# Kernel optimization log

Measured on AMD Instinct MI355X. Metric: run time of the kernel, lower is better.

## Reference

```python
import jax, jax.numpy as jnp
import numpy as np

N_NODES = 100000
N_EDGES = 3200000
DIM = 128
N_LAYERS = 3
NUM_GRAPHS = 128
BN_EPS = 1e-5
GIN_EPS = 0.0  # eps buffer initialized to 0, train_eps=False


def setup_inputs() -> dict:
    key = jax.random.key(0)
    ks = jax.random.split(key, 12)
    s = 1.0 / np.sqrt(DIM)
    inp = {
        "x": jax.random.normal(ks[0], (N_NODES, DIM), jnp.float32),
        "edge_index": jax.random.randint(ks[1], (2, N_EDGES), 0, N_NODES, jnp.int64),
        "batch": jnp.sort(jax.random.randint(ks[2], (N_NODES,), 0, NUM_GRAPHS, jnp.int64)),
        # node encoder Linear(x_dim, emb_dim)
        "W_node": jax.random.uniform(ks[3], (DIM, DIM), jnp.float32, -s, s),
        "b_node": jax.random.uniform(ks[4], (DIM,), jnp.float32, -s, s),
        # per-layer MLP: Linear -> BatchNorm -> ReLU -> Linear, stacked over layers
        "W1": jax.random.uniform(ks[5], (N_LAYERS, DIM, DIM), jnp.float32, -s, s),
        "b1": jax.random.uniform(ks[6], (N_LAYERS, DIM), jnp.float32, -s, s),
        "gamma": jnp.ones((N_LAYERS, DIM), jnp.float32),
        "beta": jnp.zeros((N_LAYERS, DIM), jnp.float32),
        "W2": jax.random.uniform(ks[7], (N_LAYERS, DIM, DIM), jnp.float32, -s, s),
        "b2": jax.random.uniform(ks[8], (N_LAYERS, DIM), jnp.float32, -s, s),
    }
    return inp


def _batchnorm(y, gamma, beta):
    # training-mode batch statistics over the node dimension (biased variance)
    mean = jnp.mean(y, axis=0)
    var = jnp.mean(jnp.square(y - mean), axis=0)
    return (y - mean) * jax.lax.rsqrt(var + BN_EPS) * gamma + beta


def reference(x, edge_index, batch, W_node, b_node, W1, b1, gamma, beta, W2, b2):
    src, dst = edge_index[0], edge_index[1]
    n = x.shape[0]
    h = x @ W_node + b_node  # [N, D]
    for i in range(N_LAYERS):
        # GINConv: scatter-add gathered neighbor features, eps-residual, MLP
        agg = jax.ops.segment_sum(h[src], dst, num_segments=n)  # [N, D]
        out = agg + (1.0 + GIN_EPS) * h
        y = out @ W1[i] + b1[i]
        y = jax.nn.relu(_batchnorm(y, gamma[i], beta[i]))
        y = y @ W2[i] + b2[i]
        h = jax.nn.relu(y)  # outer ReLU in Encoder.forward (dropout_p=0)
    # global_add_pool
    return jax.ops.segment_sum(h, batch, num_segments=NUM_GRAPHS)  # [G, D]
```

## Files before the change

kernel.cpp:

```cpp
#include <hip/hip_runtime.h>

#define N_NODES 100000
#define M_PAD   100096
#define N_EDGES 3200000
#define DIM 128
#define N_LAYERS 3
#define NUM_GRAPHS 128
#define BN_EPS 1e-5f

#define DST_SHIFT 7
#define BUCKET_NODES 128
#define N_BUCKETS ((N_NODES + BUCKET_NODES - 1) / BUCKET_NODES)
#define BUCKET_CAP 4864
#define EDGES_PER_BLOCK 16384
#define BIN_BLOCKS ((N_EDGES + EDGES_PER_BLOCK - 1) / EDGES_PER_BLOCK)
#define N_BANDS 64

#define AGG_BLOCKS 25000
#define AGG_CHUNK  (AGG_BLOCKS / 8)

typedef unsigned int uint32;
typedef unsigned short u16;
typedef __attribute__((ext_vector_type(8))) short bf16x8;
typedef __attribute__((ext_vector_type(4))) float f32x4;

__device__ __forceinline__ float bf2f(u16 u) {
    union { uint32 i; float f; } c;
    c.i = ((uint32)u) << 16;
    return c.f;
}
__device__ __forceinline__ u16 f2bf(float f) {
    union { float f; uint32 i; } c;
    c.f = f;
    uint32 i = c.i;
    return (u16)((i + 0x7FFFu + ((i >> 16) & 1u)) >> 16);
}
__device__ __forceinline__ float lo_bf(uint32 v) {
    union { uint32 i; float f; } c;
    c.i = v << 16;
    return c.f;
}
__device__ __forceinline__ float hi_bf(uint32 v) {
    union { uint32 i; float f; } c;
    c.i = v & 0xFFFF0000u;
    return c.f;
}
__device__ __forceinline__ uint32 pack_bf2(float a, float b) {
    return ((uint32)f2bf(b) << 16) | (uint32)f2bf(a);
}
__device__ __forceinline__ void unpack_add8(float* acc, uint4 v) {
    acc[0] += lo_bf(v.x); acc[1] += hi_bf(v.x);
    acc[2] += lo_bf(v.y); acc[3] += hi_bf(v.y);
    acc[4] += lo_bf(v.z); acc[5] += hi_bf(v.z);
    acc[6] += lo_bf(v.w); acc[7] += hi_bf(v.w);
}

__global__ __launch_bounds__(256) void zero_misc(int* __restrict__ gcur,
                                                 float* __restrict__ bn_stats,
                                                 float* __restrict__ outp,
                                                 uint32* __restrict__ aggpad32) {
    int i = blockIdx.x * 256 + threadIdx.x;
    if (i < N_BUCKETS) gcur[i] = 0;
    if (i < N_LAYERS * 2 * DIM) bn_stats[i] = 0.f;
    if (i < NUM_GRAPHS * DIM) outp[i] = 0.f;
    if (i < (M_PAD - N_NODES) * DIM / 2) aggpad32[i] = 0;
}

__global__ __launch_bounds__(256) void bin_by_dst(const int* __restrict__ src,
                                                  const int* __restrict__ dst,
                                                  int* __restrict__ gcur,
                                                  uint32* __restrict__ packed) {
    __shared__ int cnt[N_BUCKETS];
    __shared__ int cur[N_BUCKETS];
    int t = threadIdx.x;
    int e0 = blockIdx.x * EDGES_PER_BLOCK;
    for (int i = t; i < N_BUCKETS; i += 256) cnt[i] = 0;
    __syncthreads();

    for (int j = 0; j < EDGES_PER_BLOCK / 256; ++j) {
        int e = e0 + j * 256 + t;
        if (e < N_EDGES) atomicAdd(&cnt[dst[e] >> DST_SHIFT], 1);
    }
    __syncthreads();
    for (int i = t; i < N_BUCKETS; i += 256) {
        int c = cnt[i];
        cur[i] = c ? atomicAdd(&gcur[i], c) : 0;
    }
    __syncthreads();
    for (int j = 0; j < EDGES_PER_BLOCK / 256; ++j) {
        int e = e0 + j * 256 + t;
        if (e < N_EDGES) {
            int d = dst[e];
            int b = d >> DST_SHIFT;
            int pos = atomicAdd(&cur[b], 1);
            if (pos < BUCKET_CAP)
                packed[(size_t)b * BUCKET_CAP + pos] =
                    (uint32)src[e] | ((uint32)(d & (BUCKET_NODES - 1)) << 17);
        }
    }
}

__global__ void scan_buckets(const int* __restrict__ gcur, int* __restrict__ obase,
                             int* __restrict__ row_ptr) {
    __shared__ int s[N_BUCKETS];
    int t = threadIdx.x;
    for (int i = t; i < N_BUCKETS; i += 256) {
        int c = gcur[i];
        s[i] = (c > BUCKET_CAP) ? BUCKET_CAP : c;
    }
    __syncthreads();
    if (t == 0) {
        int run = 0;
        for (int i = 0; i < N_BUCKETS; ++i) {
            int c = s[i];
            s[i] = run;
            run += c;
        }
        row_ptr[N_NODES] = run;
    }
    __syncthreads();
    for (int i = t; i < N_BUCKETS; i += 256) obase[i] = s[i];
}

__global__ __launch_bounds__(256) void build_buckets(const uint32* __restrict__ packed,
                                                     const int* __restrict__ gcur,
                                                     const int* __restrict__ obase_arr,
                                                     int* __restrict__ row_ptr,
                                                     int* __restrict__ col_src) {
    __shared__ uint32 ed[BUCKET_CAP];
    __shared__ uint32 ed2[BUCKET_CAP];
    __shared__ int bandcur[N_BANDS];
    __shared__ int ncnt[BUCKET_NODES];
    __shared__ int ncur[BUCKET_NODES];
    int b = blockIdx.x, t = threadIdx.x;
    int cnt = gcur[b];
    if (cnt > BUCKET_CAP) cnt = BUCKET_CAP;
    int obase = obase_arr[b];
    int n0 = b * BUCKET_NODES;

    if (t < N_BANDS) bandcur[t] = 0;
    if (t < BUCKET_NODES) ncnt[t] = 0;
    __syncthreads();

    const uint32* reg = packed + (size_t)b * BUCKET_CAP;
    for (int i = t; i < cnt; i += 256) {
        uint32 v = reg[i];
        ed[i] = v;
        atomicAdd(&bandcur[(v & 0x1FFFFu) >> 11], 1);
        atomicAdd(&ncnt[v >> 17], 1);
    }
    __syncthreads();

    if (t == 0) {
        int run = 0;
        for (int w = 0; w < N_BANDS; ++w) {
            int c = bandcur[w];
            bandcur[w] = run;
            run += c;
        }
    }
    int myc = (t < BUCKET_NODES) ? ncnt[t] : 0;
    if (t < BUCKET_NODES) ncur[t] = myc;
    __syncthreads();
    for (int off = 1; off < BUCKET_NODES; off <<= 1) {
        int v = 0;
        if (t < BUCKET_NODES && t >= off) v = ncur[t - off];
        __syncthreads();
        if (t < BUCKET_NODES) ncur[t] += v;
        __syncthreads();
    }
    if (t < BUCKET_NODES) {
        int excl = ncur[t] - myc;
        ncur[t] = excl;
        int gn = n0 + t;
        if (gn < N_NODES) row_ptr[gn] = obase + excl;
    }
    __syncthreads();

    for (int i = t; i < cnt; i += 256) {
        uint32 v = ed[i];
        int p = atomicAdd(&bandcur[(v & 0x1FFFFu) >> 11], 1);
        ed2[p] = v;
    }
    __syncthreads();

    for (int i = t; i < cnt; i += 256) {
        uint32 v = ed2[i];
        int slot = atomicAdd(&ncur[v >> 17], 1);
        col_src[obase + slot] = (int)(v & 0x1FFFFu);
    }
}

__global__ void cvt_wt_all(const float* __restrict__ Wn, const float* __restrict__ W1,
                           const float* __restrict__ W2, u16* __restrict__ WT) {
    int m = blockIdx.x >> 7, n = blockIdx.x & 127, k = threadIdx.x;
    const float* src = (m == 0) ? Wn
                     : (m <= 3) ? W1 + (size_t)(m - 1) * DIM * DIM
                                : W2 + (size_t)(m - 4) * DIM * DIM;
    int L = n * 256 + k * 2;
    int Ls = L ^ ((n & 7) << 4);
    *(u16*)((char*)WT + (size_t)m * 32768 + Ls) = f2bf(src[(size_t)k * DIM + n]);
}

__global__ __launch_bounds__(256) void aggregate_bf(const u16* __restrict__ h,
                                                    const int* __restrict__ row_ptr,
                                                    const int* __restrict__ col_src,
                                                    u16* __restrict__ agg) {
    int wg = (blockIdx.x & 7) * AGG_CHUNK + (blockIdx.x >> 3);
    int wv = wg * 4 + (threadIdx.x >> 6);
    int lane = threadIdx.x & 63;
    int q = lane >> 4, c = lane & 15;
    if (wv >= N_NODES) return;
    int beg = row_ptr[wv], end = row_ptr[wv + 1];
    const uint4* h4 = (const uint4*)h;

    float acc[8];
#pragma unroll
    for (int j = 0; j < 8; ++j) acc[j] = 0.f;

    if (q == 0) {
        uint4 v = h4[(size_t)wv * 16 + c];
        unpack_add8(acc, v);
    }
    int e = beg + q;
    for (; e + 12 < end; e += 16) {
        int i0 = col_src[e];
        int i1 = col_src[e + 4];
        int i2 = col_src[e + 8];
        int i3 = col_src[e + 12];
        uint4 v0 = h4[(size_t)i0 * 16 + c];
        uint4 v1 = h4[(size_t)i1 * 16 + c];
        uint4 v2 = h4[(size_t)i2 * 16 + c];
        uint4 v3 = h4[(size_t)i3 * 16 + c];
        unpack_add8(acc, v0);
        unpack_add8(acc, v1);
        unpack_add8(acc, v2);
        unpack_add8(acc, v3);
    }
    for (; e < end; e += 4) {
        uint4 v0 = h4[(size_t)col_src[e] * 16 + c];
        unpack_add8(acc, v0);
    }
#pragma unroll
    for (int j = 0; j < 8; ++j) {
        acc[j] += __shfl_xor(acc[j], 16);
        acc[j] += __shfl_xor(acc[j], 32);
    }
    if (q == 0) {
        uint4 o;
        o.x = pack_bf2(acc[0], acc[1]);
        o.y = pack_bf2(acc[2], acc[3]);
        o.z = pack_bf2(acc[4], acc[5]);
        o.w = pack_bf2(acc[6], acc[7]);
        *(uint4*)&agg[(size_t)wv * DIM + c * 8] = o;
    }
}

template <int MODE>
__global__ __launch_bounds__(256) void gemm_v2(const void* __restrict__ Av,
                                               const u16* __restrict__ WTs,
                                               const float* __restrict__ bias,
                                               u16* __restrict__ outp,
                                               float* __restrict__ bn_sum,
                                               float* __restrict__ bn_sumsq,
                                               const float* __restrict__ gamma,
                                               const float* __restrict__ beta) {
    __shared__ u16 sB[DIM * DIM];
    __shared__ float sc_[DIM];
    __shared__ float sh_[DIM];
    __shared__ float ls[4][DIM];
    __shared__ float lq[4][DIM];

    int t = threadIdx.x;
    int wid = t >> 6, lane = t & 63;
    int hw = lane >> 4, c = lane & 15;
    int row0 = blockIdx.x * 128 + wid * 32;

    bf16x8 a[2][4];
    float4 af[2][4][2];
#pragma unroll
    for (int rf = 0; rf < 2; ++rf) {
        int row = row0 + rf * 16 + c;
#pragma unroll
        for (int ks = 0; ks < 4; ++ks) {
            int k0 = ks * 32 + hw * 8;
            if (MODE == 0) {
                const float* xf = (const float*)Av;
                af[rf][ks][0] = make_float4(0.f, 0.f, 0.f, 0.f);
                af[rf][ks][1] = af[rf][ks][0];
                if (row < N_NODES) {
                    af[rf][ks][0] = *(const float4*)&xf[(size_t)row * DIM + k0];
                    af[rf][ks][1] = *(const float4*)&xf[(size_t)row * DIM + k0 + 4];
                }
            } else {
                const u16* Ab = (const u16*)Av;
                a[rf][ks] = *(const bf16x8*)&Ab[(size_t)row * DIM + k0];
            }
        }
    }

    {
        const uint4* Wg = (const uint4*)WTs;
        uint4* sB4 = (uint4*)sB;
#pragma unroll
        for (int i = 0; i < 8; ++i) sB4[i * 256 + t] = Wg[i * 256 + t];
    }
    if (MODE == 2 && t < DIM) {
        const float invN = 1.0f / (float)N_NODES;
        float mean = bn_sum[t] * invN;
        float var = fmaxf(bn_sumsq[t] * invN - mean * mean, 0.f);
        float rs = rsqrtf(var + BN_EPS);
        float sc = gamma[t] * rs;
        sc_[t] = sc;
        sh_[t] = beta[t] - mean * sc;
    }
    __syncthreads();

#pragma unroll
    for (int rf = 0; rf < 2; ++rf) {
#pragma unroll
        for (int ks = 0; ks < 4; ++ks) {
            int k0 = ks * 32 + hw * 8;
            if (MODE == 0) {
                union { bf16x8 v; u16 u[8]; } ua;
                float4 v0 = af[rf][ks][0], v1 = af[rf][ks][1];
                ua.u[0] = f2bf(v0.x); ua.u[1] = f2bf(v0.y);
                ua.u[2] = f2bf(v0.z); ua.u[3] = f2bf(v0.w);
                ua.u[4] = f2bf(v1.x); ua.u[5] = f2bf(v1.y);
                ua.u[6] = f2bf(v1.z); ua.u[7] = f2bf(v1.w);
                a[rf][ks] = ua.v;
            } else if (MODE == 2) {
                union { bf16x8 v; u16 u[8]; } ua;
                ua.v = a[rf][ks];
#pragma unroll
                for (int j = 0; j < 8; ++j) {
                    float f = bf2f(ua.u[j]);
                    f = fmaxf(fmaf(f, sc_[k0 + j], sh_[k0 + j]), 0.f);
                    ua.u[j] = f2bf(f);
                }
                a[rf][ks] = ua.v;
            }
        }
    }

    f32x4 acc[2][8];
#pragma unroll
    for (int rf = 0; rf < 2; ++rf)
#pragma unroll
        for (int nf = 0; nf < 8; ++nf) acc[rf][nf] = (f32x4){0.f, 0.f, 0.f, 0.f};

    int swz = (c & 7) << 4;
#pragma unroll
    for (int ks = 0; ks < 4; ++ks) {
#pragma unroll
        for (int nf = 0; nf < 8; ++nf) {
            int L = (nf * 4096 + c * 256 + ks * 64 + hw * 16) ^ swz;
            bf16x8 b = *(const bf16x8*)((const char*)sB + L);
            acc[0][nf] = __builtin_amdgcn_mfma_f32_16x16x32_bf16(a[0][ks], b, acc[0][nf], 0, 0, 0);
            acc[1][nf] = __builtin_amdgcn_mfma_f32_16x16x32_bf16(a[1][ks], b, acc[1][nf], 0, 0, 0);
        }
    }

    float s_[8], q_[8];
#pragma unroll
    for (int nf = 0; nf < 8; ++nf) { s_[nf] = 0.f; q_[nf] = 0.f; }

#pragma unroll
    for (int rf = 0; rf < 2; ++rf) {
        int rbase = row0 + rf * 16 + hw * 4;
#pragma unroll
        for (int nf = 0; nf < 8; ++nf) {
            float bv = bias[nf * 16 + c];
#pragma unroll
            for (int r = 0; r < 4; ++r) {
                float v = acc[rf][nf][r] + bv;
                if (MODE == 2) v = fmaxf(v, 0.f);
                outp[(size_t)(rbase + r) * DIM + nf * 16 + c] = f2bf(v);
                if (MODE == 1) {
                    float m = (rbase + r < N_NODES) ? v : 0.f;
                    s_[nf] += m;
                    q_[nf] += m * m;
                }
            }
        }
    }

    if (MODE == 1) {
#pragma unroll
        for (int nf = 0; nf < 8; ++nf) {
            s_[nf] += __shfl_xor(s_[nf], 16);
            s_[nf] += __shfl_xor(s_[nf], 32);
            q_[nf] += __shfl_xor(q_[nf], 16);
            q_[nf] += __shfl_xor(q_[nf], 32);
        }
        if (lane < 16) {
#pragma unroll
            for (int nf = 0; nf < 8; ++nf) {
                ls[wid][nf * 16 + c] = s_[nf];
                lq[wid][nf * 16 + c] = q_[nf];
            }
        }
        __syncthreads();
        if (t < DIM) {
            atomicAdd(&bn_sum[t], ls[0][t] + ls[1][t] + ls[2][t] + ls[3][t]);
            atomicAdd(&bn_sumsq[t], lq[0][t] + lq[1][t] + lq[2][t] + lq[3][t]);
        }
    }
}

__global__ __launch_bounds__(256) void pool_bf(const u16* __restrict__ h,
                                               const int* __restrict__ batch,
                                               float* __restrict__ out) {
    int wv = (blockIdx.x * 256 + threadIdx.x) >> 6;
    int lane = threadIdx.x & 63;
    int base = wv * 32;
    if (base >= N_NODES) return;
    int end = base + 32;
    if (end > N_NODES) end = N_NODES;
    const uint32* h32 = (const uint32*)h;
    float ax = 0.f, ay = 0.f;
    int curg = batch[base];
    for (int n = base; n < end; ++n) {
        int g = batch[n];
        if (g != curg) {
            atomicAdd(&out[curg * DIM + lane * 2], ax);
            atomicAdd(&out[curg * DIM + lane * 2 + 1], ay);
            ax = 0.f;
            ay = 0.f;
            curg = g;
        }
        uint32 v = h32[(size_t)n * 64 + lane];
        ax += lo_bf(v);
        ay += hi_bf(v);
    }
    atomicAdd(&out[curg * DIM + lane * 2], ax);
    atomicAdd(&out[curg * DIM + lane * 2 + 1], ay);
}

extern "C" void kernel_launch(void* const* d_in, const int* in_sizes, int n_in,
                              void* d_out, int out_size, void* d_ws, size_t ws_size,
                              hipStream_t stream) {
    const float* x     = (const float*)d_in[0];
    const int*   ei    = (const int*)d_in[1];
    const int*   batch = (const int*)d_in[2];
    const float* Wn    = (const float*)d_in[3];
    const float* bnode = (const float*)d_in[4];
    const float* W1    = (const float*)d_in[5];
    const float* b1    = (const float*)d_in[6];
    const float* gamma = (const float*)d_in[7];
    const float* beta  = (const float*)d_in[8];
    const float* W2    = (const float*)d_in[9];
    const float* b2    = (const float*)d_in[10];
    float* out = (float*)d_out;

    const int* e_src = ei;
    const int* e_dst = ei + N_EDGES;

    const size_t MD = (size_t)M_PAD * DIM;
    u16* h   = (u16*)d_ws;
    u16* agg = h + MD;
    u16* y   = agg + MD;
    u16* WT  = y + MD;
    int* row_ptr = (int*)(WT + 7 * DIM * DIM);
    int* col_src = row_ptr + N_NODES + 1;
    int* gcur    = col_src + N_EDGES;
    int* obase   = gcur + N_BUCKETS;
    float* bn_stats = (float*)(obase + N_BUCKETS);
    uint32* packed = (uint32*)y;

    const int GEMM_BLOCKS = M_PAD / 128;
    const int POOL_BLOCKS = (((N_NODES + 31) / 32) * 64 + 255) / 256;

    zero_misc<<<64, 256, 0, stream>>>(gcur, bn_stats, out,
                                      (uint32*)(agg + (size_t)N_NODES * DIM));
    bin_by_dst<<<BIN_BLOCKS, 256, 0, stream>>>(e_src, e_dst, gcur, packed);
    scan_buckets<<<1, 256, 0, stream>>>(gcur, obase, row_ptr);
    build_buckets<<<N_BUCKETS, 256, 0, stream>>>(packed, gcur, obase, row_ptr, col_src);

    cvt_wt_all<<<7 * DIM, DIM, 0, stream>>>(Wn, W1, W2, WT);

    gemm_v2<0><<<GEMM_BLOCKS, 256, 0, stream>>>(x, WT, bnode, h, nullptr,
                                                nullptr, nullptr, nullptr);

    for (int i = 0; i < N_LAYERS; ++i) {
        float* bn_sum = bn_stats + (size_t)i * 2 * DIM;
        float* bn_sumsq = bn_sum + DIM;
        aggregate_bf<<<AGG_BLOCKS, 256, 0, stream>>>(h, row_ptr, col_src, agg);
        gemm_v2<1><<<GEMM_BLOCKS, 256, 0, stream>>>(
            agg, WT + (size_t)(1 + i) * DIM * DIM, b1 + i * DIM, y, bn_sum,
            bn_sumsq, nullptr, nullptr);
        gemm_v2<2><<<GEMM_BLOCKS, 256, 0, stream>>>(
            y, WT + (size_t)(4 + i) * DIM * DIM, b2 + i * DIM, h, bn_sum,
            bn_sumsq, gamma + i * DIM, beta + i * DIM);
    }

    pool_bf<<<POOL_BLOCKS, 256, 0, stream>>>(h, batch, out);
}
```

Baseline: 611.2 us.

## Fuse global add pool into final GEMM epilogue and parallelize bucket scan

The last layer's second GEMM now accumulates ReLU outputs directly into per-graph pool sums using shared-memory slots for up to 8 graphs per block, with a global-atomic fallback. This removes the separate pool kernel and the write and read-back of the final h. The single-threaded serial prefix scan over buckets is replaced with a wave-shuffle parallel scan. The cost is shared-memory atomics inside the GEMM epilogue, which may contend, and more global atomics when a block spans many graphs.

```diff
diff --git a/kernel.cpp b/kernel.cpp
--- a/kernel.cpp
+++ b/kernel.cpp
@@ -100,26 +100,43 @@
     }
 }
 
-__global__ void scan_buckets(const int* __restrict__ gcur, int* __restrict__ obase,
-                             int* __restrict__ row_ptr) {
-    __shared__ int s[N_BUCKETS];
+__global__ __launch_bounds__(256) void scan_buckets(const int* __restrict__ gcur,
+                                                    int* __restrict__ obase,
+                                                    int* __restrict__ row_ptr) {
     int t = threadIdx.x;
-    for (int i = t; i < N_BUCKETS; i += 256) {
-        int c = gcur[i];
-        s[i] = (c > BUCKET_CAP) ? BUCKET_CAP : c;
-    }
-    __syncthreads();
-    if (t == 0) {
-        int run = 0;
-        for (int i = 0; i < N_BUCKETS; ++i) {
-            int c = s[i];
-            s[i] = run;
-            run += c;
-        }
-        row_ptr[N_NODES] = run;
-    }
-    __syncthreads();
-    for (int i = t; i < N_BUCKETS; i += 256) obase[i] = s[i];
+    int lane = t & 63, wid = t >> 6;
+    int v[4];
+    int sum = 0;
+#pragma unroll
+    for (int j = 0; j < 4; ++j) {
+        int idx = t * 4 + j;
+        int c = 0;
+        if (idx < N_BUCKETS) {
+            c = gcur[idx];
+            if (c > BUCKET_CAP) c = BUCKET_CAP;
+        }
+        v[j] = c;
+        sum += c;
+    }
+    int x = sum;
+#pragma unroll
+    for (int off = 1; off < 64; off <<= 1) {
+        int y = __shfl_up(x, off);
+        if (lane >= off) x += y;
+    }
+    __shared__ int wsum[4];
+    if (lane == 63) wsum[wid] = x;
+    __syncthreads();
+    int wexcl = 0;
+    for (int w = 0; w < wid; ++w) wexcl += wsum[w];
+    int run = wexcl + (x - sum);
+#pragma unroll
+    for (int j = 0; j < 4; ++j) {
+        int idx = t * 4 + j;
+        if (idx < N_BUCKETS) obase[idx] = run;
+        run += v[j];
+    }
+    if (t == 255) row_ptr[N_NODES] = run;
 }
 
 __global__ __launch_bounds__(256) void build_buckets(const uint32* __restrict__ packed,
@@ -257,19 +274,20 @@
 }
 
 template <int MODE>
-__global__ __launch_bounds__(256) void gemm_v2(const void* __restrict__ Av,
+__global__ __launch_bounds__(256) void gemm_v3(const void* __restrict__ Av,
                                                const u16* __restrict__ WTs,
                                                const float* __restrict__ bias,
                                                u16* __restrict__ outp,
                                                float* __restrict__ bn_sum,
                                                float* __restrict__ bn_sumsq,
                                                const float* __restrict__ gamma,
-                                               const float* __restrict__ beta) {
+                                               const float* __restrict__ beta,
+                                               const int* __restrict__ batchp,
+                                               float* __restrict__ poolout) {
     __shared__ u16 sB[DIM * DIM];
     __shared__ float sc_[DIM];
     __shared__ float sh_[DIM];
-    __shared__ float ls[4][DIM];
-    __shared__ float lq[4][DIM];
+    __shared__ float lsq[8][DIM];
 
     int t = threadIdx.x;
     int wid = t >> 6, lane = t & 63;
@@ -305,7 +323,7 @@
 #pragma unroll
         for (int i = 0; i < 8; ++i) sB4[i * 256 + t] = Wg[i * 256 + t];
     }
-    if (MODE == 2 && t < DIM) {
+    if ((MODE == 2 || MODE == 3) && t < DIM) {
         const float invN = 1.0f / (float)N_NODES;
         float mean = bn_sum[t] * invN;
         float var = fmaxf(bn_sumsq[t] * invN - mean * mean, 0.f);
@@ -313,6 +331,9 @@
         float sc = gamma[t] * rs;
         sc_[t] = sc;
         sh_[t] = beta[t] - mean * sc;
+    }
+    if (MODE == 3) {
+        for (int i = t; i < 8 * DIM; i += 256) ((float*)lsq)[i] = 0.f;
     }
     __syncthreads();
 
@@ -329,7 +350,7 @@
                 ua.u[4] = f2bf(v1.x); ua.u[5] = f2bf(v1.y);
                 ua.u[6] = f2bf(v1.z); ua.u[7] = f2bf(v1.w);
                 a[rf][ks] = ua.v;
-            } else if (MODE == 2) {
+            } else if (MODE == 2 || MODE == 3) {
                 union { bf16x8 v; u16 u[8]; } ua;
                 ua.v = a[rf][ks];
 #pragma unroll
@@ -365,6 +386,21 @@
 #pragma unroll
     for (int nf = 0; nf < 8; ++nf) { s_[nf] = 0.f; q_[nf] = 0.f; }
 
+    int gmin = 0;
+    int gg[2][4];
+    if (MODE == 3) {
+        gmin = batchp[blockIdx.x * 128];
+#pragma unroll
+        for (int rf = 0; rf < 2; ++rf) {
+            int rbase = row0 + rf * 16 + hw * 4;
+#pragma unroll
+            for (int r = 0; r < 4; ++r) {
+                int row = rbase + r;
+                gg[rf][r] = (row < N_NODES) ? (batchp[row] - gmin) : -1;
+            }
+        }
+    }
+
 #pragma unroll
     for (int rf = 0; rf < 2; ++rf) {
         int rbase = row0 + rf * 16 + hw * 4;
@@ -374,12 +410,22 @@
 #pragma unroll
             for (int r = 0; r < 4; ++r) {
                 float v = acc[rf][nf][r] + bv;
-                if (MODE == 2) v = fmaxf(v, 0.f);
-                outp[(size_t)(rbase + r) * DIM + nf * 16 + c] = f2bf(v);
-                if (MODE == 1) {
-                    float m = (rbase + r < N_NODES) ? v : 0.f;
-                    s_[nf] += m;
-                    q_[nf] += m * m;
+                if (MODE == 2 || MODE == 3) v = fmaxf(v, 0.f);
+                if (MODE == 3) {
+                    int s = gg[rf][r];
+                    if (s >= 0) {
+                        if (s < 8)
+                            atomicAdd(&lsq[s][nf * 16 + c], v);
+                        else
+                            atomicAdd(&poolout[(gmin + s) * DIM + nf * 16 + c], v);
+                    }
+                } else {
+                    outp[(size_t)(rbase + r) * DIM + nf * 16 + c] = f2bf(v);
+                    if (MODE == 1) {
+                        float m = (rbase + r < N_NODES) ? v : 0.f;
+                        s_[nf] += m;
+                        q_[nf] += m * m;
+                    }
                 }
             }
         }
@@ -396,45 +442,27 @@
         if (lane < 16) {
 #pragma unroll
             for (int nf = 0; nf < 8; ++nf) {
-                ls[wid][nf * 16 + c] = s_[nf];
-                lq[wid][nf * 16 + c] = q_[nf];
+                lsq[wid][nf * 16 + c] = s_[nf];
+                lsq[4 + wid][nf * 16 + c] = q_[nf];
             }
         }
         __syncthreads();
         if (t < DIM) {
-            atomicAdd(&bn_sum[t], ls[0][t] + ls[1][t] + ls[2][t] + ls[3][t]);
-            atomicAdd(&bn_sumsq[t], lq[0][t] + lq[1][t] + lq[2][t] + lq[3][t]);
-        }
-    }
-}
-
-__global__ __launch_bounds__(256) void pool_bf(const u16* __restrict__ h,
-                                               const int* __restrict__ batch,
-                                               float* __restrict__ out) {
-    int wv = (blockIdx.x * 256 + threadIdx.x) >> 6;
-    int lane = threadIdx.x & 63;
-    int base = wv * 32;
-    if (base >= N_NODES) return;
-    int end = base + 32;
-    if (end > N_NODES) end = N_NODES;
-    const uint32* h32 = (const uint32*)h;
-    float ax = 0.f, ay = 0.f;
-    int curg = batch[base];
-    for (int n = base; n < end; ++n) {
-        int g = batch[n];
-        if (g != curg) {
-            atomicAdd(&out[curg * DIM + lane * 2], ax);
-            atomicAdd(&out[curg * DIM + lane * 2 + 1], ay);
-            ax = 0.f;
-            ay = 0.f;
-            curg = g;
-        }
-        uint32 v = h32[(size_t)n * 64 + lane];
-        ax += lo_bf(v);
-        ay += hi_bf(v);
-    }
-    atomicAdd(&out[curg * DIM + lane * 2], ax);
-    atomicAdd(&out[curg * DIM + lane * 2 + 1], ay);
+            atomicAdd(&bn_sum[t], lsq[0][t] + lsq[1][t] + lsq[2][t] + lsq[3][t]);
+            atomicAdd(&bn_sumsq[t], lsq[4][t] + lsq[5][t] + lsq[6][t] + lsq[7][t]);
+        }
+    }
+
+    if (MODE == 3) {
+        __syncthreads();
+        for (int i = t; i < 8 * DIM; i += 256) {
+            float v = ((float*)lsq)[i];
+            if (v != 0.f) {
+                int slot = i >> 7, col = i & 127;
+                atomicAdd(&poolout[(gmin + slot) * DIM + col], v);
+            }
+        }
+    }
 }
 
 extern "C" void kernel_launch(void* const* d_in, const int* in_sizes, int n_in,
@@ -469,7 +497,6 @@
     uint32* packed = (uint32*)y;
 
     const int GEMM_BLOCKS = M_PAD / 128;
-    const int POOL_BLOCKS = (((N_NODES + 31) / 32) * 64 + 255) / 256;
 
     zero_misc<<<64, 256, 0, stream>>>(gcur, bn_stats, out,
                                       (uint32*)(agg + (size_t)N_NODES * DIM));
@@ -479,20 +506,25 @@
 
     cvt_wt_all<<<7 * DIM, DIM, 0, stream>>>(Wn, W1, W2, WT);
 
-    gemm_v2<0><<<GEMM_BLOCKS, 256, 0, stream>>>(x, WT, bnode, h, nullptr,
-                                                nullptr, nullptr, nullptr);
+    gemm_v3<0><<<GEMM_BLOCKS, 256, 0, stream>>>(x, WT, bnode, h, nullptr,
+                                                nullptr, nullptr, nullptr,
+                                                nullptr, nullptr);
 
     for (int i = 0; i < N_LAYERS; ++i) {
         float* bn_sum = bn_stats + (size_t)i * 2 * DIM;
         float* bn_sumsq = bn_sum + DIM;
         aggregate_bf<<<AGG_BLOCKS, 256, 0, stream>>>(h, row_ptr, col_src, agg);
-        gemm_v2<1><<<GEMM_BLOCKS, 256, 0, stream>>>(
+        gemm_v3<1><<<GEMM_BLOCKS, 256, 0, stream>>>(
             agg, WT + (size_t)(1 + i) * DIM * DIM, b1 + i * DIM, y, bn_sum,
-            bn_sumsq, nullptr, nullptr);
-        gemm_v2<2><<<GEMM_BLOCKS, 256, 0, stream>>>(
-            y, WT + (size_t)(4 + i) * DIM * DIM, b2 + i * DIM, h, bn_sum,
-            bn_sumsq, gamma + i * DIM, beta + i * DIM);
-    }
-
-    pool_bf<<<POOL_BLOCKS, 256, 0, stream>>>(h, batch, out);
-}
+            bn_sumsq, nullptr, nullptr, nullptr, nullptr);
+        if (i < N_LAYERS - 1) {
+            gemm_v3<2><<<GEMM_BLOCKS, 256, 0, stream>>>(
+                y, WT + (size_t)(4 + i) * DIM * DIM, b2 + i * DIM, h, bn_sum,
+                bn_sumsq, gamma + i * DIM, beta + i * DIM, nullptr, nullptr);
+        } else {
+            gemm_v3<3><<<GEMM_BLOCKS, 256, 0, stream>>>(
+                y, WT + (size_t)(4 + i) * DIM * DIM, b2 + i * DIM, nullptr,
+                bn_sum, bn_sumsq, gamma + i * DIM, beta + i * DIM, batch, out);
+        }
+    }
+}
```

After: 664.0 us. 8.6% more time.
